# Kernel optimization log

Hardware: AMD Instinct MI355X
Metric: run time of the kernel (lower is better)

Reference implementation:

```python
import jax, jax.numpy as jnp
import numpy as np

B = 16      # number of point clouds in the batch
N = 2048    # points per cloud
P = B * N   # total points (flat PyG-style batching)
K = 16      # neighbors per point (col 0 = self loop)
OUT = 512   # out_channels


def _linear(key, fi, fo):
    # torch nn.Linear default init: U(-1/sqrt(fi), 1/sqrt(fi))
    s = 1.0 / np.sqrt(fi)
    kw, kb = jax.random.split(key)
    W = jax.random.uniform(kw, (fi, fo), jnp.float32, -s, s)
    b = jax.random.uniform(kb, (fo,), jnp.float32, -s, s)
    return W, b


def setup_inputs() -> dict:
    key = jax.random.key(0)
    ks = jax.random.split(key, 6)
    pos = jax.random.normal(ks[0], (P, 3), jnp.float32)
    # flat batch vector: points are grouped contiguously per cloud
    batch = (jnp.arange(P, dtype=jnp.int32) // N).astype(jnp.int32)
    # within-cloud random neighbor indices (stand-in for knn/radius graph)
    base = (jnp.arange(P) // N) * N  # offset of each point's cloud
    nbr = base[:, None] + jax.random.randint(ks[1], (P, K), 0, N)
    nbr = nbr.at[:, 0].set(jnp.arange(P))  # self loop (PyG add_self_loops)
    W1, b1 = _linear(ks[2], 3, 64)          # sa1 MLP layer 1
    W2, b2 = _linear(ks[3], 64, 128)        # sa1 MLP layer 2
    W3, b3 = _linear(ks[4], 128 + 3, 256)   # sa2 MLP layer 1
    W4, b4 = _linear(ks[5], 256, OUT)       # sa2 MLP layer 2
    return dict(pos=pos, nbr=nbr.astype(jnp.int64), batch=batch,
                W1=W1, b1=b1, W2=W2, b2=b2, W3=W3, b3=b3, W4=W4, b4=b4)


def reference(pos, nbr, batch, W1, b1, W2, b2, W3, b3, W4, b4):
    # ----- sa1: x is None -> message = MLP(pos_j - pos_i), max-aggregated -----
    diff = pos[nbr] - pos[:, None, :]                      # [P, K, 3]
    h1 = jnp.maximum(diff @ W1 + b1, 0.0) @ W2 + b2        # [P, K, 128]
    x1 = jnp.max(h1, axis=1)                               # [P, 128]
    # ----- sa2: message = MLP([x1_j, pos_j - pos_i]), max-aggregated -----
    feats = jnp.concatenate([x1[nbr], diff], axis=-1)      # [P, K, 131]
    h2 = jnp.maximum(feats @ W3 + b3, 0.0) @ W4 + b4       # [P, K, 512]
    x2 = jnp.max(h2, axis=1)                               # [P, 512]
    # ----- global_max_pool over batch -----
    return jax.ops.segment_max(x2, batch, num_segments=B)  # [B, 512]
```

## Files before the change

kernel.cpp:

```cpp
#include <hip/hip_runtime.h>
#include <hip/hip_bf16.h>

#define PTOT   32768
#define KNB    16
#define NCLOUD 16
#define OUTC   512
#define A1S    168
#define A2S    264

typedef __attribute__((ext_vector_type(8)))  short v8bf;
typedef __attribute__((ext_vector_type(16))) float v16f;

__device__ __forceinline__ unsigned short f2b(float v) {
    __hip_bfloat16 h = __float2bfloat16(v);
    return *reinterpret_cast<unsigned short*>(&h);
}
__device__ __forceinline__ unsigned pk2(float a, float b) {
    return (unsigned)f2b(a) | ((unsigned)f2b(b) << 16);
}
__device__ __forceinline__ unsigned fenc(float f) {
    unsigned u = __float_as_uint(f);
    return (u & 0x80000000u) ? ~u : (u | 0x80000000u);
}
__device__ __forceinline__ float fdec(unsigned u) {
    unsigned b = (u & 0x80000000u) ? (u & 0x7FFFFFFFu) : ~u;
    return __uint_as_float(b);
}
__device__ __forceinline__ v16f zero16() {
    v16f z;
    #pragma unroll
    for (int i = 0; i < 16; ++i) z[i] = 0.0f;
    return z;
}

__global__ __launch_bounds__(256) void sa1_kernel(
    const float* __restrict__ pos, const int* __restrict__ nbr,
    const float* __restrict__ W1, const float* __restrict__ b1,
    const float* __restrict__ W2, const float* __restrict__ b2,
    const float* __restrict__ W3, const float* __restrict__ W4,
    unsigned short* __restrict__ W3s, unsigned short* __restrict__ W4s,
    unsigned* __restrict__ encbuf,
    unsigned short* __restrict__ x1b)
{
    __shared__ unsigned short A1d[256 * 16];
    __shared__ unsigned short A2[256 * 72];
    const int tid  = threadIdx.x;
    const int lane = tid & 63;
    const int wave = tid >> 6;
    const int l31  = lane & 31;
    const int h    = lane >> 5;

    {
        const int b = blockIdx.x;
        if (b < 32) {
            #pragma unroll
            for (int it = 0; it < 16; ++it) {
                int e = tid + it * 256;
                int jj = e >> 9, n = e & 511;
                A1d[e] = f2b(W4[(b * 8 + jj) * 512 + n]);
            }
            __syncthreads();
            #pragma unroll
            for (int it = 0; it < 16; ++it) {
                int o = tid + it * 256;
                W4s[b * 4096 + o] = A1d[(o & 7) * 512 + (o >> 3)];
            }
            __syncthreads();
        } else if (b < 50) {
            int c2 = b - 32;
            #pragma unroll
            for (int it = 0; it < 8; ++it) {
                int e = tid + it * 256;
                int jj = e >> 8, n = e & 255;
                int k = c2 * 8 + jj;
                A1d[e] = f2b(k < 131 ? W3[k * 256 + n] : 0.0f);
            }
            __syncthreads();
            #pragma unroll
            for (int it = 0; it < 8; ++it) {
                int o = tid + it * 256;
                W3s[c2 * 2048 + o] = A1d[(o & 7) * 256 + (o >> 3)];
            }
            __syncthreads();
        }
        if (b == 2047) {
            for (int i = tid; i < NCLOUD * OUTC; i += 256) encbuf[i] = 0u;
        }
    }

    const int c1 = (wave >> 1) * 32 + l31;
    v8bf b1f;
    #pragma unroll
    for (int i = 0; i < 8; ++i) b1f[i] = 0;
    if (h == 0) {
        b1f[0] = (short)f2b(W1[c1]);
        b1f[1] = (short)f2b(W1[64 + c1]);
        b1f[2] = (short)f2b(W1[128 + c1]);
    }
    const float b1v = b1[c1];
    const int cW2 = wave * 32 + l31;
    v8bf B2[4];
    #pragma unroll
    for (int kc = 0; kc < 4; ++kc)
        #pragma unroll
        for (int j = 0; j < 8; ++j)
            B2[kc][j] = (short)f2b(W2[(kc * 16 + h * 8 + j) * 128 + cW2]);
    const float b2v = b2[cW2];

    const int p0 = blockIdx.x * 16;

    {
        int r = tid;
        int j = nbr[p0 * KNB + r];
        int p = p0 + (r >> 4);
        v8bf z;
        #pragma unroll
        for (int i = 0; i < 8; ++i) z[i] = 0;
        v8bf dv = z;
        dv[0] = (short)f2b(pos[j * 3 + 0] - pos[p * 3 + 0]);
        dv[1] = (short)f2b(pos[j * 3 + 1] - pos[p * 3 + 1]);
        dv[2] = (short)f2b(pos[j * 3 + 2] - pos[p * 3 + 2]);
        *(v8bf*)(A1d + r * 16)     = dv;
        *(v8bf*)(A1d + r * 16 + 8) = z;
    }
    __syncthreads();

    #pragma unroll
    for (int rr = 0; rr < 4; ++rr) {
        const int rt = (wave & 1) + rr * 2;
        v8bf a = *(const v8bf*)(A1d + (rt * 32 + l31) * 16 + h * 8);
        v16f acc = __builtin_amdgcn_mfma_f32_32x32x16_bf16(a, b1f, zero16(), 0, 0, 0);
        #pragma unroll
        for (int r = 0; r < 16; ++r) {
            int row = rt * 32 + (r & 3) + 8 * (r >> 2) + 4 * h;
            A2[row * 72 + c1] = f2b(fmaxf(acc[r] + b1v, 0.0f));
        }
    }
    __syncthreads();

    #pragma unroll
    for (int rt = 0; rt < 8; ++rt) {
        v16f acc = zero16();
        #pragma unroll
        for (int kc = 0; kc < 4; ++kc) {
            v8bf a = *(const v8bf*)(A2 + (rt * 32 + l31) * 72 + kc * 16 + h * 8);
            acc = __builtin_amdgcn_mfma_f32_32x32x16_bf16(a, B2[kc], acc, 0, 0, 0);
        }
        float ma = acc[0], mb = acc[8];
        #pragma unroll
        for (int r = 1; r < 8; ++r) { ma = fmaxf(ma, acc[r]); mb = fmaxf(mb, acc[8 + r]); }
        ma = fmaxf(ma, __shfl_xor(ma, 32));
        mb = fmaxf(mb, __shfl_xor(mb, 32));
        int p = p0 + rt * 2 + h;
        float m = h ? mb : ma;
        x1b[p * 128 + cW2] = f2b(m + b2v);
    }
}

__global__ __launch_bounds__(256, 2) void sa2_kernel(
    const float* __restrict__ pos, const int* __restrict__ nbr,
    const int* __restrict__ batch,
    const unsigned short* __restrict__ W3s, const float* __restrict__ b3,
    const unsigned short* __restrict__ W4s, const float* __restrict__ b4,
    const unsigned short* __restrict__ x1b, unsigned* __restrict__ encbuf)
{
    __shared__ unsigned short S[128 * A2S];
    const int tid  = threadIdx.x;
    const int lane = tid & 63;
    const int wave = tid >> 6;
    const int l31  = lane & 31;
    const int h    = lane >> 5;
    const int p0   = blockIdx.x * 8;

    const float b3v0 = b3[(wave * 2 + 0) * 32 + l31];
    const float b3v1 = b3[(wave * 2 + 1) * 32 + l31];

    {
        int r = tid >> 1, q = tid & 1;
        int j = nbr[p0 * KNB + r];
        const uint4* src = (const uint4*)(x1b + j * 128 + q * 64);
        uint4* dst = (uint4*)(S + r * A1S + q * 64);
        #pragma unroll
        for (int i = 0; i < 8; ++i) dst[i] = src[i];
    }
    if (tid < 128) {
        int r = tid;
        int j = nbr[p0 * KNB + r];
        int p = p0 + (r >> 4);
        v8bf z;
        #pragma unroll
        for (int i = 0; i < 8; ++i) z[i] = 0;
        v8bf dv = z;
        dv[0] = (short)f2b(pos[j * 3 + 0] - pos[p * 3 + 0]);
        dv[1] = (short)f2b(pos[j * 3 + 1] - pos[p * 3 + 1]);
        dv[2] = (short)f2b(pos[j * 3 + 2] - pos[p * 3 + 2]);
        *(v8bf*)(S + r * A1S + 128) = dv;
        *(v8bf*)(S + r * A1S + 136) = z;
    }
    __syncthreads();

    const int n1a = (wave * 2 + 0) * 32 + l31;
    const int n1b = (wave * 2 + 1) * 32 + l31;
    unsigned stA[2][16], stB[2][16];
    #pragma unroll
    for (int rtp = 0; rtp < 2; ++rtp) {
        v16f g00 = zero16(), g01 = zero16(), g10 = zero16(), g11 = zero16();
        #pragma unroll
        for (int kc = 0; kc < 9; ++kc) {
            v8bf a0 = *(const v8bf*)(S + (rtp * 64 + l31)      * A1S + kc * 16 + h * 8);
            v8bf a1 = *(const v8bf*)(S + (rtp * 64 + 32 + l31) * A1S + kc * 16 + h * 8);
            int c2 = kc * 2 + h;
            v8bf B0 = *(const v8bf*)(W3s + ((c2 * 256 + n1a) << 3));
            v8bf B1 = *(const v8bf*)(W3s + ((c2 * 256 + n1b) << 3));
            g00 = __builtin_amdgcn_mfma_f32_32x32x16_bf16(a0, B0, g00, 0, 0, 0);
            g10 = __builtin_amdgcn_mfma_f32_32x32x16_bf16(a1, B0, g10, 0, 0, 0);
            g01 = __builtin_amdgcn_mfma_f32_32x32x16_bf16(a0, B1, g01, 0, 0, 0);
            g11 = __builtin_amdgcn_mfma_f32_32x32x16_bf16(a1, B1, g11, 0, 0, 0);
        }
        #pragma unroll
        for (int i = 0; i < 8; ++i) {
            stA[rtp][i]     = pk2(fmaxf(g00[2*i] + b3v0, 0.0f), fmaxf(g00[2*i+1] + b3v0, 0.0f));
            stA[rtp][8 + i] = pk2(fmaxf(g10[2*i] + b3v0, 0.0f), fmaxf(g10[2*i+1] + b3v0, 0.0f));
            stB[rtp][i]     = pk2(fmaxf(g01[2*i] + b3v1, 0.0f), fmaxf(g01[2*i+1] + b3v1, 0.0f));
            stB[rtp][8 + i] = pk2(fmaxf(g11[2*i] + b3v1, 0.0f), fmaxf(g11[2*i+1] + b3v1, 0.0f));
        }
    }

    const int ct0_0 = wave * 4;
    const int n0_0 = ct0_0 * 32 + l31;
    const int n1_0 = (ct0_0 + 1) * 32 + l31;
    v8bf B2a[16], B2b[16];
    #pragma unroll
    for (int kc = 0; kc < 16; ++kc) {
        int c2 = kc * 2 + h;
        B2a[kc] = *(const v8bf*)(W4s + ((c2 * 512 + n0_0) << 3));
        B2b[kc] = *(const v8bf*)(W4s + ((c2 * 512 + n1_0) << 3));
    }

    __syncthreads();

    {
        const int c0 = (wave * 2 + 0) * 32 + l31;
        const int c1 = (wave * 2 + 1) * 32 + l31;
        #pragma unroll
        for (int rtp = 0; rtp < 2; ++rtp) {
            const int rb = rtp * 64;
            #pragma unroll
            for (int i = 0; i < 8; ++i) {
                int row = rb + ((2*i) & 3) + 8 * ((2*i) >> 2) + 4 * h;
                S[row * A2S + c0]        = (unsigned short)(stA[rtp][i] & 0xFFFF);
                S[(row + 1) * A2S + c0]  = (unsigned short)(stA[rtp][i] >> 16);
                S[(row + 32) * A2S + c0] = (unsigned short)(stA[rtp][8 + i] & 0xFFFF);
                S[(row + 33) * A2S + c0] = (unsigned short)(stA[rtp][8 + i] >> 16);
                S[row * A2S + c1]        = (unsigned short)(stB[rtp][i] & 0xFFFF);
                S[(row + 1) * A2S + c1]  = (unsigned short)(stB[rtp][i] >> 16);
                S[(row + 32) * A2S + c1] = (unsigned short)(stB[rtp][8 + i] & 0xFFFF);
                S[(row + 33) * A2S + c1] = (unsigned short)(stB[rtp][8 + i] >> 16);
            }
        }
    }
    __syncthreads();

    const int cloud = batch[p0];
    {
        float rm0 = -3.4e38f, rm1 = -3.4e38f;
        #pragma unroll
        for (int rtp = 0; rtp < 2; ++rtp) {
            v16f a00 = zero16(), a01 = zero16(), a10 = zero16(), a11 = zero16();
            #pragma unroll
            for (int kc = 0; kc < 16; ++kc) {
                v8bf a0 = *(const v8bf*)(S + (rtp * 64 + l31)      * A2S + kc * 16 + h * 8);
                v8bf a1 = *(const v8bf*)(S + (rtp * 64 + 32 + l31) * A2S + kc * 16 + h * 8);
                a00 = __builtin_amdgcn_mfma_f32_32x32x16_bf16(a0, B2a[kc], a00, 0, 0, 0);
                a10 = __builtin_amdgcn_mfma_f32_32x32x16_bf16(a1, B2a[kc], a10, 0, 0, 0);
                a01 = __builtin_amdgcn_mfma_f32_32x32x16_bf16(a0, B2b[kc], a01, 0, 0, 0);
                a11 = __builtin_amdgcn_mfma_f32_32x32x16_bf16(a1, B2b[kc], a11, 0, 0, 0);
            }
            #pragma unroll
            for (int r = 0; r < 16; ++r) {
                rm0 = fmaxf(rm0, fmaxf(a00[r], a10[r]));
                rm1 = fmaxf(rm1, fmaxf(a01[r], a11[r]));
            }
        }
        rm0 = fmaxf(rm0, __shfl_xor(rm0, 32));
        rm1 = fmaxf(rm1, __shfl_xor(rm1, 32));
        rm0 += b4[ct0_0 * 32 + l31];
        rm1 += b4[(ct0_0 + 1) * 32 + l31];
        if (lane < 32) {
            atomicMax(&encbuf[cloud * OUTC + ct0_0 * 32 + l31], fenc(rm0));
            atomicMax(&encbuf[cloud * OUTC + (ct0_0 + 1) * 32 + l31], fenc(rm1));
        }
    }

    {
        const int ct0 = wave * 4 + 2;
        const int n0 = ct0 * 32 + l31;
        const int n1 = (ct0 + 1) * 32 + l31;
        #pragma unroll
        for (int kc = 0; kc < 16; ++kc) {
            int c2 = kc * 2 + h;
            B2a[kc] = *(const v8bf*)(W4s + ((c2 * 512 + n0) << 3));
            B2b[kc] = *(const v8bf*)(W4s + ((c2 * 512 + n1) << 3));
        }
        float rm0 = -3.4e38f, rm1 = -3.4e38f;
        #pragma unroll
        for (int rtp = 0; rtp < 2; ++rtp) {
            v16f a00 = zero16(), a01 = zero16(), a10 = zero16(), a11 = zero16();
            #pragma unroll
            for (int kc = 0; kc < 16; ++kc) {
                v8bf a0 = *(const v8bf*)(S + (rtp * 64 + l31)      * A2S + kc * 16 + h * 8);
                v8bf a1 = *(const v8bf*)(S + (rtp * 64 + 32 + l31) * A2S + kc * 16 + h * 8);
                a00 = __builtin_amdgcn_mfma_f32_32x32x16_bf16(a0, B2a[kc], a00, 0, 0, 0);
                a10 = __builtin_amdgcn_mfma_f32_32x32x16_bf16(a1, B2a[kc], a10, 0, 0, 0);
                a01 = __builtin_amdgcn_mfma_f32_32x32x16_bf16(a0, B2b[kc], a01, 0, 0, 0);
                a11 = __builtin_amdgcn_mfma_f32_32x32x16_bf16(a1, B2b[kc], a11, 0, 0, 0);
            }
            #pragma unroll
            for (int r = 0; r < 16; ++r) {
                rm0 = fmaxf(rm0, fmaxf(a00[r], a10[r]));
                rm1 = fmaxf(rm1, fmaxf(a01[r], a11[r]));
            }
        }
        rm0 = fmaxf(rm0, __shfl_xor(rm0, 32));
        rm1 = fmaxf(rm1, __shfl_xor(rm1, 32));
        rm0 += b4[ct0 * 32 + l31];
        rm1 += b4[(ct0 + 1) * 32 + l31];
        if (lane < 32) {
            atomicMax(&encbuf[cloud * OUTC + ct0 * 32 + l31], fenc(rm0));
            atomicMax(&encbuf[cloud * OUTC + (ct0 + 1) * 32 + l31], fenc(rm1));
        }
    }
}

__global__ void finalize_kernel(const unsigned* __restrict__ encv,
                                float* __restrict__ out)
{
    int i = blockIdx.x * 256 + threadIdx.x;
    if (i < NCLOUD * OUTC) out[i] = fdec(encv[i]);
}

extern "C" void kernel_launch(void* const* d_in, const int* in_sizes, int n_in,
                              void* d_out, int out_size, void* d_ws, size_t ws_size,
                              hipStream_t stream)
{
    const float* pos   = (const float*)d_in[0];
    const int*   nbr   = (const int*)  d_in[1];
    const int*   batch = (const int*)  d_in[2];
    const float* W1    = (const float*)d_in[3];
    const float* b1    = (const float*)d_in[4];
    const float* W2    = (const float*)d_in[5];
    const float* b2    = (const float*)d_in[6];
    const float* W3    = (const float*)d_in[7];
    const float* b3    = (const float*)d_in[8];
    const float* W4    = (const float*)d_in[9];
    const float* b4    = (const float*)d_in[10];

    unsigned short* x1b = (unsigned short*)d_ws;
    unsigned short* W3s = (unsigned short*)((char*)d_ws + 8388608);
    unsigned short* W4s = (unsigned short*)((char*)d_ws + 8470528);
    unsigned*    encbuf = (unsigned*)((char*)d_ws + 8732672);

    sa1_kernel<<<PTOT / 16, 256, 0, stream>>>(pos, nbr, W1, b1, W2, b2, W3, W4,
                                              W3s, W4s, encbuf, x1b);
    sa2_kernel<<<PTOT / 8, 256, 0, stream>>>(pos, nbr, batch, W3s, b3, W4s, b4,
                                             x1b, encbuf);
    finalize_kernel<<<(NCLOUD * OUTC + 255) / 256, 256, 0, stream>>>(encbuf, (float*)d_out);
}
```

Baseline: 266.4 us.

## Precompute per-point x1·W3 projection and gather it per edge in sa2

```diff
diff --git a/kernel.cpp b/kernel.cpp
--- a/kernel.cpp
+++ b/kernel.cpp
@@ -14,6 +14,9 @@
 __device__ __forceinline__ unsigned short f2b(float v) {
     __hip_bfloat16 h = __float2bfloat16(v);
     return *reinterpret_cast<unsigned short*>(&h);
+}
+__device__ __forceinline__ float b2f(unsigned short u) {
+    return __uint_as_float(((unsigned)u) << 16);
 }
 __device__ __forceinline__ unsigned pk2(float a, float b) {
     return (unsigned)f2b(a) | ((unsigned)f2b(b) << 16);
@@ -157,7 +160,150 @@
     }
 }
 
-__global__ __launch_bounds__(256, 2) void sa2_kernel(
+__global__ __launch_bounds__(256) void ymap_kernel(
+    const unsigned short* __restrict__ x1b,
+    const unsigned short* __restrict__ W3s,
+    const float* __restrict__ b3,
+    unsigned short* __restrict__ y)
+{
+    __shared__ unsigned short X[128 * 128];
+    const int tid  = threadIdx.x;
+    const int lane = tid & 63;
+    const int wave = tid >> 6;
+    const int l31  = lane & 31;
+    const int h    = lane >> 5;
+    const int p0   = blockIdx.x * 128;
+
+    {
+        int r = tid >> 1, q = tid & 1;
+        const uint4* src = (const uint4*)(x1b + (p0 + r) * 128 + q * 64);
+        uint4* dst = (uint4*)(X + r * 128 + q * 64);
+        #pragma unroll
+        for (int i = 0; i < 8; ++i) dst[i] = src[i];
+    }
+    __syncthreads();
+
+    #pragma unroll
+    for (int ci = 0; ci < 2; ++ci) {
+        const int ct = wave * 2 + ci;
+        const int n  = ct * 32 + l31;
+        v8bf Bf[8];
+        #pragma unroll
+        for (int kc = 0; kc < 8; ++kc)
+            Bf[kc] = *(const v8bf*)(W3s + (((kc * 2 + h) * 256 + n) << 3));
+        const float b3v = b3[n];
+        v16f a0 = zero16(), a1 = zero16(), a2 = zero16(), a3 = zero16();
+        #pragma unroll
+        for (int kc = 0; kc < 8; ++kc) {
+            v8bf x0 = *(const v8bf*)(X + (0 * 32 + l31) * 128 + kc * 16 + h * 8);
+            v8bf x1 = *(const v8bf*)(X + (1 * 32 + l31) * 128 + kc * 16 + h * 8);
+            v8bf x2 = *(const v8bf*)(X + (2 * 32 + l31) * 128 + kc * 16 + h * 8);
+            v8bf x3 = *(const v8bf*)(X + (3 * 32 + l31) * 128 + kc * 16 + h * 8);
+            a0 = __builtin_amdgcn_mfma_f32_32x32x16_bf16(x0, Bf[kc], a0, 0, 0, 0);
+            a1 = __builtin_amdgcn_mfma_f32_32x32x16_bf16(x1, Bf[kc], a1, 0, 0, 0);
+            a2 = __builtin_amdgcn_mfma_f32_32x32x16_bf16(x2, Bf[kc], a2, 0, 0, 0);
+            a3 = __builtin_amdgcn_mfma_f32_32x32x16_bf16(x3, Bf[kc], a3, 0, 0, 0);
+        }
+        #pragma unroll
+        for (int r = 0; r < 16; ++r) {
+            int cr = (r & 3) + 8 * (r >> 2) + 4 * h;
+            y[(p0 + 0  + cr) * 256 + n] = f2b(a0[r] + b3v);
+            y[(p0 + 32 + cr) * 256 + n] = f2b(a1[r] + b3v);
+            y[(p0 + 64 + cr) * 256 + n] = f2b(a2[r] + b3v);
+            y[(p0 + 96 + cr) * 256 + n] = f2b(a3[r] + b3v);
+        }
+    }
+}
+
+__global__ __launch_bounds__(256) void sa2y_kernel(
+    const float* __restrict__ pos, const int* __restrict__ nbr,
+    const int* __restrict__ batch,
+    const float* __restrict__ W3,
+    const unsigned short* __restrict__ W4s, const float* __restrict__ b4,
+    const unsigned short* __restrict__ y, unsigned* __restrict__ encbuf)
+{
+    __shared__ unsigned short S[128 * A2S];
+    const int tid  = threadIdx.x;
+    const int lane = tid & 63;
+    const int wave = tid >> 6;
+    const int l31  = lane & 31;
+    const int h    = lane >> 5;
+    const int p0   = blockIdx.x * 8;
+
+    {
+        const int r  = tid & 127;
+        const int qq = __builtin_amdgcn_readfirstlane(wave >> 1);
+        const int j  = nbr[p0 * KNB + r];
+        const int p  = p0 + (r >> 4);
+        const float d0 = pos[j * 3 + 0] - pos[p * 3 + 0];
+        const float d1 = pos[j * 3 + 1] - pos[p * 3 + 1];
+        const float d2 = pos[j * 3 + 2] - pos[p * 3 + 2];
+        const float* W3d = W3 + 128 * 256;
+        #pragma unroll
+        for (int c = 0; c < 16; ++c) {
+            const int n0 = qq * 128 + c * 8;
+            v8bf yv = *(const v8bf*)(y + j * 256 + n0);
+            float se[8];
+            #pragma unroll
+            for (int e = 0; e < 8; ++e) {
+                float s = b2f((unsigned short)yv[e])
+                        + d0 * W3d[n0 + e]
+                        + d1 * W3d[256 + n0 + e]
+                        + d2 * W3d[512 + n0 + e];
+                se[e] = fmaxf(s, 0.0f);
+            }
+            uint4 u;
+            u.x = pk2(se[0], se[1]); u.y = pk2(se[2], se[3]);
+            u.z = pk2(se[4], se[5]); u.w = pk2(se[6], se[7]);
+            *reinterpret_cast<uint4*>(S + r * A2S + n0) = u;
+        }
+    }
+    __syncthreads();
+
+    const int cloud = batch[p0];
+    #pragma unroll
+    for (int cp = 0; cp < 2; ++cp) {
+        const int ct0 = wave * 4 + cp * 2;
+        const int n0 = ct0 * 32 + l31;
+        const int n1 = (ct0 + 1) * 32 + l31;
+        v8bf B2a[16], B2b[16];
+        #pragma unroll
+        for (int kc = 0; kc < 16; ++kc) {
+            int c2 = kc * 2 + h;
+            B2a[kc] = *(const v8bf*)(W4s + ((c2 * 512 + n0) << 3));
+            B2b[kc] = *(const v8bf*)(W4s + ((c2 * 512 + n1) << 3));
+        }
+        float rm0 = -3.4e38f, rm1 = -3.4e38f;
+        #pragma unroll
+        for (int rtp = 0; rtp < 2; ++rtp) {
+            v16f a00 = zero16(), a01 = zero16(), a10 = zero16(), a11 = zero16();
+            #pragma unroll
+            for (int kc = 0; kc < 16; ++kc) {
+                v8bf a0 = *(const v8bf*)(S + (rtp * 64 + l31)      * A2S + kc * 16 + h * 8);
+                v8bf a1 = *(const v8bf*)(S + (rtp * 64 + 32 + l31) * A2S + kc * 16 + h * 8);
+                a00 = __builtin_amdgcn_mfma_f32_32x32x16_bf16(a0, B2a[kc], a00, 0, 0, 0);
+                a10 = __builtin_amdgcn_mfma_f32_32x32x16_bf16(a1, B2a[kc], a10, 0, 0, 0);
+                a01 = __builtin_amdgcn_mfma_f32_32x32x16_bf16(a0, B2b[kc], a01, 0, 0, 0);
+                a11 = __builtin_amdgcn_mfma_f32_32x32x16_bf16(a1, B2b[kc], a11, 0, 0, 0);
+            }
+            #pragma unroll
+            for (int r = 0; r < 16; ++r) {
+                rm0 = fmaxf(rm0, fmaxf(a00[r], a10[r]));
+                rm1 = fmaxf(rm1, fmaxf(a01[r], a11[r]));
+            }
+        }
+        rm0 = fmaxf(rm0, __shfl_xor(rm0, 32));
+        rm1 = fmaxf(rm1, __shfl_xor(rm1, 32));
+        rm0 += b4[ct0 * 32 + l31];
+        rm1 += b4[(ct0 + 1) * 32 + l31];
+        if (lane < 32) {
+            atomicMax(&encbuf[cloud * OUTC + ct0 * 32 + l31], fenc(rm0));
+            atomicMax(&encbuf[cloud * OUTC + (ct0 + 1) * 32 + l31], fenc(rm1));
+        }
+    }
+}
+
+__global__ __launch_bounds__(256) void sa2_kernel(
     const float* __restrict__ pos, const int* __restrict__ nbr,
     const int* __restrict__ batch,
     const unsigned short* __restrict__ W3s, const float* __restrict__ b3,
@@ -225,18 +371,6 @@
             stB[rtp][8 + i] = pk2(fmaxf(g11[2*i] + b3v1, 0.0f), fmaxf(g11[2*i+1] + b3v1, 0.0f));
         }
     }
-
-    const int ct0_0 = wave * 4;
-    const int n0_0 = ct0_0 * 32 + l31;
-    const int n1_0 = (ct0_0 + 1) * 32 + l31;
-    v8bf B2a[16], B2b[16];
-    #pragma unroll
-    for (int kc = 0; kc < 16; ++kc) {
-        int c2 = kc * 2 + h;
-        B2a[kc] = *(const v8bf*)(W4s + ((c2 * 512 + n0_0) << 3));
-        B2b[kc] = *(const v8bf*)(W4s + ((c2 * 512 + n1_0) << 3));
-    }
-
     __syncthreads();
 
     {
@@ -262,40 +396,12 @@
     __syncthreads();
 
     const int cloud = batch[p0];
-    {
-        float rm0 = -3.4e38f, rm1 = -3.4e38f;
-        #pragma unroll
-        for (int rtp = 0; rtp < 2; ++rtp) {
-            v16f a00 = zero16(), a01 = zero16(), a10 = zero16(), a11 = zero16();
-            #pragma unroll
-            for (int kc = 0; kc < 16; ++kc) {
-                v8bf a0 = *(const v8bf*)(S + (rtp * 64 + l31)      * A2S + kc * 16 + h * 8);
-                v8bf a1 = *(const v8bf*)(S + (rtp * 64 + 32 + l31) * A2S + kc * 16 + h * 8);
-                a00 = __builtin_amdgcn_mfma_f32_32x32x16_bf16(a0, B2a[kc], a00, 0, 0, 0);
-                a10 = __builtin_amdgcn_mfma_f32_32x32x16_bf16(a1, B2a[kc], a10, 0, 0, 0);
-                a01 = __builtin_amdgcn_mfma_f32_32x32x16_bf16(a0, B2b[kc], a01, 0, 0, 0);
-                a11 = __builtin_amdgcn_mfma_f32_32x32x16_bf16(a1, B2b[kc], a11, 0, 0, 0);
-            }
-            #pragma unroll
-            for (int r = 0; r < 16; ++r) {
-                rm0 = fmaxf(rm0, fmaxf(a00[r], a10[r]));
-                rm1 = fmaxf(rm1, fmaxf(a01[r], a11[r]));
-            }
-        }
-        rm0 = fmaxf(rm0, __shfl_xor(rm0, 32));
-        rm1 = fmaxf(rm1, __shfl_xor(rm1, 32));
-        rm0 += b4[ct0_0 * 32 + l31];
-        rm1 += b4[(ct0_0 + 1) * 32 + l31];
-        if (lane < 32) {
-            atomicMax(&encbuf[cloud * OUTC + ct0_0 * 32 + l31], fenc(rm0));
-            atomicMax(&encbuf[cloud * OUTC + (ct0_0 + 1) * 32 + l31], fenc(rm1));
-        }
-    }
-
-    {
-        const int ct0 = wave * 4 + 2;
+    #pragma unroll
+    for (int cp = 0; cp < 2; ++cp) {
+        const int ct0 = wave * 4 + cp * 2;
         const int n0 = ct0 * 32 + l31;
         const int n1 = (ct0 + 1) * 32 + l31;
+        v8bf B2a[16], B2b[16];
         #pragma unroll
         for (int kc = 0; kc < 16; ++kc) {
             int c2 = kc * 2 + h;
@@ -355,14 +461,31 @@
     const float* W4    = (const float*)d_in[9];
     const float* b4    = (const float*)d_in[10];
 
-    unsigned short* x1b = (unsigned short*)d_ws;
-    unsigned short* W3s = (unsigned short*)((char*)d_ws + 8388608);
-    unsigned short* W4s = (unsigned short*)((char*)d_ws + 8470528);
-    unsigned*    encbuf = (unsigned*)((char*)d_ws + 8732672);
-
-    sa1_kernel<<<PTOT / 16, 256, 0, stream>>>(pos, nbr, W1, b1, W2, b2, W3, W4,
-                                              W3s, W4s, encbuf, x1b);
-    sa2_kernel<<<PTOT / 8, 256, 0, stream>>>(pos, nbr, batch, W3s, b3, W4s, b4,
-                                             x1b, encbuf);
-    finalize_kernel<<<(NCLOUD * OUTC + 255) / 256, 256, 0, stream>>>(encbuf, (float*)d_out);
-}
+    const size_t NEED = 16777216UL + 8388608UL + 81920UL + 262144UL + 32768UL;
+
+    if (ws_size >= NEED) {
+        unsigned short* y   = (unsigned short*)d_ws;
+        unsigned short* x1b = (unsigned short*)((char*)d_ws + 16777216);
+        unsigned short* W3s = (unsigned short*)((char*)d_ws + 25165824);
+        unsigned short* W4s = (unsigned short*)((char*)d_ws + 25247744);
+        unsigned*    encbuf = (unsigned*)((char*)d_ws + 25509888);
+
+        sa1_kernel<<<PTOT / 16, 256, 0, stream>>>(pos, nbr, W1, b1, W2, b2, W3, W4,
+                                                  W3s, W4s, encbuf, x1b);
+        ymap_kernel<<<PTOT / 128, 256, 0, stream>>>(x1b, W3s, b3, y);
+        sa2y_kernel<<<PTOT / 8, 256, 0, stream>>>(pos, nbr, batch, W3,
+                                                  W4s, b4, y, encbuf);
+        finalize_kernel<<<(NCLOUD * OUTC + 255) / 256, 256, 0, stream>>>(encbuf, (float*)d_out);
+    } else {
+        unsigned short* x1b = (unsigned short*)d_ws;
+        unsigned short* W3s = (unsigned short*)((char*)d_ws + 8388608);
+        unsigned short* W4s = (unsigned short*)((char*)d_ws + 8470528);
+        unsigned*    encbuf = (unsigned*)((char*)d_ws + 8732672);
+
+        sa1_kernel<<<PTOT / 16, 256, 0, stream>>>(pos, nbr, W1, b1, W2, b2, W3, W4,
+                                                  W3s, W4s, encbuf, x1b);
+        sa2_kernel<<<PTOT / 8, 256, 0, stream>>>(pos, nbr, batch, W3s, b3, W4s, b4,
+                                                 x1b, encbuf);
+        finalize_kernel<<<(NCLOUD * OUTC + 255) / 256, 256, 0, stream>>>(encbuf, (float*)d_out);
+    }
+}
```

Measured after the change: 272.6 us. +2.4%, slower.
